# Optimization experiments

Measured on AMD Instinct MI355X. Metric: run time of the kernel, lower is better.

Reference implementation:

```python
import jax, jax.numpy as jnp
import numpy as np

HEAD_SIZE = 64
SCALE = HEAD_SIZE ** -0.5


def setup_inputs() -> dict:
    key = jax.random.key(0)
    ks = jax.random.split(key, 7)
    B, T, E, H = 32, 2048, 1024, HEAD_SIZE
    x = jax.random.normal(ks[0], (B, T, E), dtype=jnp.float32)
    Wq = jax.random.normal(ks[1], (E, H), dtype=jnp.float32) * (E ** -0.5)
    bq = jax.random.normal(ks[2], (H,), dtype=jnp.float32) * 0.02
    Wk = jax.random.normal(ks[3], (E, H), dtype=jnp.float32) * (E ** -0.5)
    bk = jax.random.normal(ks[4], (H,), dtype=jnp.float32) * 0.02
    Wv = jax.random.normal(ks[5], (E, H), dtype=jnp.float32) * (E ** -0.5)
    bv = jax.random.normal(ks[6], (H,), dtype=jnp.float32) * 0.02
    return {"x": x, "Wq": Wq, "bq": bq, "Wk": Wk, "bk": bk, "Wv": Wv, "bv": bv}


def reference(x, Wq, bq, Wk, bk, Wv, bv):
    # Faithful to the torch source: the tril buffer is all ones so the mask is a
    # no-op, and F.softmax's result is discarded. Output = (Q K^T * scale) @ V.
    Q = x @ Wq + bq          # [B, T, H]
    K = x @ Wk + bk          # [B, T, H]
    V = x @ Wv + bv          # [B, T, H]
    wei = jnp.einsum('bqh,bkh->bqk', Q, K) * SCALE  # [B, T, T]
    return jnp.einsum('bqk,bkh->bqh', wei, V)       # [B, T, H]
```

## Files before the change

kernel.cpp:

```cpp
#include <hip/hip_runtime.h>
#include <hip/hip_bf16.h>


using bf16x8 = __attribute__((ext_vector_type(8))) short;
using f32x4  = __attribute__((ext_vector_type(4))) float;
using u32x4  = __attribute__((ext_vector_type(4))) unsigned int;
using u32x2  = __attribute__((ext_vector_type(2))) unsigned int;
using u16    = unsigned short;

__device__ __forceinline__ u16 f2bf(float f) {
    unsigned u = __builtin_bit_cast(unsigned, f);
    u += 0x7fffu + ((u >> 16) & 1u);
    return (u16)(u >> 16);
}

#define G2L16(g, l) __builtin_amdgcn_global_load_lds(                         \
    (const __attribute__((address_space(1))) void*)(g),                       \
    (__attribute__((address_space(3))) void*)(l), 16, 0, 0)

__global__ __launch_bounds__(256) void k_wt(const float* __restrict__ Wq,
                                            const float* __restrict__ Wk,
                                            const float* __restrict__ Wv,
                                            u16* __restrict__ WT) {
    __shared__ float Wl[64][68];
    const int seg = blockIdx.x >> 4, chunk = blockIdx.x & 15;
    const float* W = (seg == 0) ? Wq : (seg == 1) ? Wk : Wv;
    const int e0 = chunk * 64;
    const int tid = threadIdx.x;
    const int lr = tid >> 4, lc = (tid & 15) * 4;
#pragma unroll
    for (int p = 0; p < 4; ++p)
        *(f32x4*)&Wl[lr + p * 16][lc] = *(const f32x4*)(W + (size_t)(e0 + lr + p * 16) * 64 + lc);
    __syncthreads();
    const int c = tid >> 2, eb = (tid & 3) * 16;
    u32x4 o0, o1;
#pragma unroll
    for (int q = 0; q < 4; ++q)
        o0[q] = (unsigned)f2bf(Wl[eb + 2 * q][c]) | ((unsigned)f2bf(Wl[eb + 2 * q + 1][c]) << 16);
#pragma unroll
    for (int q = 0; q < 4; ++q)
        o1[q] = (unsigned)f2bf(Wl[eb + 8 + 2 * q][c]) | ((unsigned)f2bf(Wl[eb + 9 + 2 * q][c]) << 16);
    u16* dst = WT + (size_t)(seg * 64 + c) * 1024 + e0 + eb;
    *(u32x4*)dst = o0;
    *(u32x4*)(dst + 8) = o1;
}

__global__ __launch_bounds__(512, 4) void k_qkv(const float* __restrict__ x,
                                                const u16* __restrict__ WT,
                                                const float* __restrict__ bq,
                                                const float* __restrict__ bk,
                                                const float* __restrict__ bv,
                                                u16* __restrict__ Qb,
                                                float* __restrict__ part) {
    __shared__ __align__(16) char lds[81920];
    const int tid  = threadIdx.x;
    const int wave = tid >> 6, lane = tid & 63;
    const int wr = wave >> 2, wc = wave & 3;
    const size_t row0 = (size_t)blockIdx.x * 64;

    size_t xsrc[2]; int xdst[2];
#pragma unroll
    for (int i = 0; i < 2; ++i) {
        const int r  = (tid >> 4) + i * 32;
        const int cb = ((tid & 15) * 16) ^ ((r & 7) << 5);
        xsrc[i] = (row0 + r) * 1024 + (cb >> 2);
        xdst[i] = i * 8192 + wave * 1024;
    }
    size_t wsrc[3]; int wdst[3];
#pragma unroll
    for (int j = 0; j < 3; ++j) {
        const int n  = (tid >> 3) + j * 64;
        const int cb = ((tid & 7) * 16) ^ ((n & 7) << 4);
        wsrc[j] = (size_t)n * 1024 + (cb >> 1);
        wdst[j] = 16384 + j * 8192 + wave * 1024;
    }

    f32x4 acc[2][3];
#pragma unroll
    for (int m = 0; m < 2; ++m)
#pragma unroll
        for (int n = 0; n < 3; ++n)
#pragma unroll
            for (int r = 0; r < 4; ++r) acc[m][n][r] = 0.0f;

#pragma unroll
    for (int i = 0; i < 2; ++i) G2L16(x + xsrc[i], lds + xdst[i]);
#pragma unroll
    for (int j = 0; j < 3; ++j) G2L16(WT + wsrc[j], lds + wdst[j]);

    for (int kc = 0; kc < 16; ++kc) {
        const int cur = kc & 1;
        if (kc < 15) {
            const int k0 = (kc + 1) * 64;
            char* base = lds + (cur ^ 1) * 40960;
#pragma unroll
            for (int i = 0; i < 2; ++i) G2L16(x + xsrc[i] + k0, base + xdst[i]);
#pragma unroll
            for (int j = 0; j < 3; ++j) G2L16(WT + wsrc[j] + k0, base + wdst[j]);
            asm volatile("s_waitcnt vmcnt(5)" ::: "memory");
        } else {
            asm volatile("s_waitcnt vmcnt(0)" ::: "memory");
        }
        __builtin_amdgcn_s_barrier();
        __builtin_amdgcn_sched_barrier(0);

        const char* xb = lds + cur * 40960;
        const char* wb = xb + 16384;
#pragma unroll
        for (int ks = 0; ks < 2; ++ks) {
            bf16x8 af[2];
#pragma unroll
            for (int m = 0; m < 2; ++m) {
                const int r = wr * 32 + m * 16 + (lane & 15);
                const int P = (r * 256 + ks * 128 + (lane >> 4) * 32) ^ ((r & 7) << 5);
                const f32x4 lo = *(const f32x4*)(xb + P);
                const f32x4 hi = *(const f32x4*)(xb + P + 16);
                u32x4 pk;
                pk[0] = (unsigned)f2bf(lo[0]) | ((unsigned)f2bf(lo[1]) << 16);
                pk[1] = (unsigned)f2bf(lo[2]) | ((unsigned)f2bf(lo[3]) << 16);
                pk[2] = (unsigned)f2bf(hi[0]) | ((unsigned)f2bf(hi[1]) << 16);
                pk[3] = (unsigned)f2bf(hi[2]) | ((unsigned)f2bf(hi[3]) << 16);
                af[m] = __builtin_bit_cast(bf16x8, pk);
            }
#pragma unroll
            for (int n = 0; n < 3; ++n) {
                const int nn = wc * 48 + n * 16 + (lane & 15);
                const int P  = (nn * 128 + ks * 64 + (lane >> 4) * 16) ^ ((nn & 7) << 4);
                const bf16x8 bfr = *(const bf16x8*)(wb + P);
                acc[0][n] = __builtin_amdgcn_mfma_f32_16x16x32_bf16(af[0], bfr, acc[0][n], 0, 0, 0);
                acc[1][n] = __builtin_amdgcn_mfma_f32_16x16x32_bf16(af[1], bfr, acc[1][n], 0, 0, 0);
            }
        }
        __builtin_amdgcn_sched_barrier(0);
        __builtin_amdgcn_s_barrier();
    }

    u16* const Kt = (u16*)lds;
    u16* const Vt = (u16*)(lds + 16384);
#pragma unroll
    for (int n = 0; n < 3; ++n) {
        const int ncol = wc * 48 + n * 16;
        const int seg = ncol >> 6;
        const int col = (ncol & 63) + (lane & 15);
        const float bias = ((seg == 0) ? bq : (seg == 1) ? bk : bv)[col];
#pragma unroll
        for (int m = 0; m < 2; ++m) {
            const int rloc = wr * 32 + m * 16 + ((lane >> 4) << 2);
            if (seg == 0) {
#pragma unroll
                for (int rr = 0; rr < 4; ++rr)
                    Qb[(row0 + rloc + rr) * 64 + col] = f2bf(acc[m][n][rr] + bias);
            } else {
                u16* const T = (seg == 1) ? Kt : Vt;
#pragma unroll
                for (int rr = 0; rr < 4; ++rr)
                    T[col * 72 + rloc + rr] = f2bf(acc[m][n][rr] + bias);
            }
        }
    }
    __syncthreads();

    float* const P = part + (size_t)blockIdx.x * 4096;
#pragma unroll
    for (int i = 0; i < 2; ++i) {
        const int f = wave * 2 + i;
        const int m0 = (f & 3) * 16;
        const int n0 = (f >> 2) * 16;
        f32x4 d;
        d[0] = d[1] = d[2] = d[3] = 0.0f;
#pragma unroll
        for (int ks = 0; ks < 2; ++ks) {
            const bf16x8 a = *(const bf16x8*)(Vt + (m0 + (lane & 15)) * 72 + ks * 32 + (lane >> 4) * 8);
            const bf16x8 b = *(const bf16x8*)(Kt + (n0 + (lane & 15)) * 72 + ks * 32 + (lane >> 4) * 8);
            d = __builtin_amdgcn_mfma_f32_16x16x32_bf16(a, b, d, 0, 0, 0);
        }
#pragma unroll
        for (int rr = 0; rr < 4; ++rr)
            P[(m0 + (lane >> 4) * 4 + rr) * 64 + n0 + (lane & 15)] = d[rr];
    }
}

__global__ __launch_bounds__(256) void k_red(const float* __restrict__ part,
                                             u16* __restrict__ KtVT) {
    const int b = blockIdx.x >> 2;
    const int o0 = (blockIdx.x & 3) * 1024 + threadIdx.x * 4;
    const float* const Pb = part + (size_t)b * 32 * 4096;
    f32x4 s;
    s[0] = s[1] = s[2] = s[3] = 0.0f;
#pragma unroll 8
    for (int c = 0; c < 32; ++c) s += *(const f32x4*)(Pb + c * 4096 + o0);
    s *= 0.125f;
    u32x2 pk;
    pk[0] = (unsigned)f2bf(s[0]) | ((unsigned)f2bf(s[1]) << 16);
    pk[1] = (unsigned)f2bf(s[2]) | ((unsigned)f2bf(s[3]) << 16);
    *(u32x2*)(KtVT + (size_t)b * 4096 + o0) = pk;
}

__global__ __launch_bounds__(256) void k_out(const u16* __restrict__ Qb,
                                             const u16* __restrict__ KtVT,
                                             float* __restrict__ out) {
    const int tid = threadIdx.x;
    const int wave = tid >> 6, lane = tid & 63;
    const size_t m0 = (size_t)blockIdx.x * 64 + wave * 16;
    const int b = blockIdx.x >> 5;
    const u16* const Bp = KtVT + (size_t)b * 4096;

    bf16x8 bfrag[2][4];
#pragma unroll
    for (int ks = 0; ks < 2; ++ks)
#pragma unroll
        for (int nt = 0; nt < 4; ++nt)
            bfrag[ks][nt] = *(const bf16x8*)(Bp + (nt * 16 + (lane & 15)) * 64 + ks * 32 + (lane >> 4) * 8);

    f32x4 acc[4];
#pragma unroll
    for (int nt = 0; nt < 4; ++nt)
#pragma unroll
        for (int r = 0; r < 4; ++r) acc[nt][r] = 0.0f;

#pragma unroll
    for (int ks = 0; ks < 2; ++ks) {
        const bf16x8 a = *(const bf16x8*)(Qb + (m0 + (lane & 15)) * 64 + ks * 32 + (lane >> 4) * 8);
#pragma unroll
        for (int nt = 0; nt < 4; ++nt)
            acc[nt] = __builtin_amdgcn_mfma_f32_16x16x32_bf16(a, bfrag[ks][nt], acc[nt], 0, 0, 0);
    }
#pragma unroll
    for (int nt = 0; nt < 4; ++nt)
#pragma unroll
        for (int rr = 0; rr < 4; ++rr)
            out[(m0 + (lane >> 4) * 4 + rr) * 64 + nt * 16 + (lane & 15)] = acc[nt][rr];
}

extern "C" void kernel_launch(void* const* d_in, const int* in_sizes, int n_in,
                              void* d_out, int out_size, void* d_ws, size_t ws_size,
                              hipStream_t stream) {
    (void)in_sizes; (void)n_in; (void)out_size; (void)ws_size;
    const float* x  = (const float*)d_in[0];
    const float* Wq = (const float*)d_in[1];
    const float* bq = (const float*)d_in[2];
    const float* Wk = (const float*)d_in[3];
    const float* bk = (const float*)d_in[4];
    const float* Wv = (const float*)d_in[5];
    const float* bv = (const float*)d_in[6];
    float* out = (float*)d_out;

    char* ws = (char*)d_ws;
    u16*  WT   = (u16*)(ws);
    u16*  Qb   = (u16*)(ws + 0x60000);
    float* part= (float*)(ws + 0x860000);
    u16*  KtVT = (u16*)(ws + 0x1860000);

    k_wt <<<48,   256, 0, stream>>>(Wq, Wk, Wv, WT);
    k_qkv<<<1024, 512, 0, stream>>>(x, WT, bq, bk, bv, Qb, part);
    k_red<<<128,  256, 0, stream>>>(part, KtVT);
    k_out<<<1024, 256, 0, stream>>>(Qb, KtVT, out);
}
```

Before: 92.33 us.

## Convert x to bf16 once in registers before staging in LDS for QKV GEMM

Rewrites the QKV projection mainloop so x is loaded into registers as fp32, converted to bf16 once, and stored into a larger bf16 LDS tile covering 256 K elements. This replaces fp32 staging via global_load_lds that re-converted each A fragment on every use. Weight tiles keep their own double-buffered async loads with adjusted waitcnts. LDS grows to 112 KB and occupancy drops to 2 blocks per CU, and the x loads are now synchronous register loads that need careful wait scheduling.

```diff
diff --git a/kernel.cpp b/kernel.cpp
--- a/kernel.cpp
+++ b/kernel.cpp
@@ -45,34 +45,30 @@
     *(u32x4*)(dst + 8) = o1;
 }
 
-__global__ __launch_bounds__(512, 4) void k_qkv(const float* __restrict__ x,
+__global__ __launch_bounds__(512, 2) void k_qkv(const float* __restrict__ x,
                                                 const u16* __restrict__ WT,
                                                 const float* __restrict__ bq,
                                                 const float* __restrict__ bk,
                                                 const float* __restrict__ bv,
                                                 u16* __restrict__ Qb,
                                                 float* __restrict__ part) {
-    __shared__ __align__(16) char lds[81920];
+    __shared__ __align__(16) char lds[114688];
     const int tid  = threadIdx.x;
     const int wave = tid >> 6, lane = tid & 63;
     const int wr = wave >> 2, wc = wave & 3;
     const size_t row0 = (size_t)blockIdx.x * 64;
 
-    size_t xsrc[2]; int xdst[2];
-#pragma unroll
-    for (int i = 0; i < 2; ++i) {
-        const int r  = (tid >> 4) + i * 32;
-        const int cb = ((tid & 15) * 16) ^ ((r & 7) << 5);
-        xsrc[i] = (row0 + r) * 1024 + (cb >> 2);
-        xdst[i] = i * 8192 + wave * 1024;
-    }
-    size_t wsrc[3]; int wdst[3];
+    const int xrow = tid >> 3;
+    const int xcs  = tid & 7;
+    const float* const xrowp = x + (row0 + xrow) * 1024 + xcs * 4;
+
+    size_t wsrc[3]; int wdstl[3];
 #pragma unroll
     for (int j = 0; j < 3; ++j) {
         const int n  = (tid >> 3) + j * 64;
         const int cb = ((tid & 7) * 16) ^ ((n & 7) << 4);
         wsrc[j] = (size_t)n * 1024 + (cb >> 1);
-        wdst[j] = 16384 + j * 8192 + wave * 1024;
+        wdstl[j] = j * 8192 + wave * 1024;
     }
 
     f32x4 acc[2][3];
@@ -83,56 +79,87 @@
 #pragma unroll
             for (int r = 0; r < 4; ++r) acc[m][n][r] = 0.0f;
 
-#pragma unroll
-    for (int i = 0; i < 2; ++i) G2L16(x + xsrc[i], lds + xdst[i]);
-#pragma unroll
-    for (int j = 0; j < 3; ++j) G2L16(WT + wsrc[j], lds + wdst[j]);
-
-    for (int kc = 0; kc < 16; ++kc) {
-        const int cur = kc & 1;
-        if (kc < 15) {
-            const int k0 = (kc + 1) * 64;
-            char* base = lds + (cur ^ 1) * 40960;
-#pragma unroll
-            for (int i = 0; i < 2; ++i) G2L16(x + xsrc[i] + k0, base + xdst[i]);
-#pragma unroll
-            for (int j = 0; j < 3; ++j) G2L16(WT + wsrc[j] + k0, base + wdst[j]);
-            asm volatile("s_waitcnt vmcnt(5)" ::: "memory");
-        } else {
-            asm volatile("s_waitcnt vmcnt(0)" ::: "memory");
-        }
-        __builtin_amdgcn_s_barrier();
-        __builtin_amdgcn_sched_barrier(0);
-
-        const char* xb = lds + cur * 40960;
-        const char* wb = xb + 16384;
-#pragma unroll
-        for (int ks = 0; ks < 2; ++ks) {
-            bf16x8 af[2];
-#pragma unroll
-            for (int m = 0; m < 2; ++m) {
-                const int r = wr * 32 + m * 16 + (lane & 15);
-                const int P = (r * 256 + ks * 128 + (lane >> 4) * 32) ^ ((r & 7) << 5);
-                const f32x4 lo = *(const f32x4*)(xb + P);
-                const f32x4 hi = *(const f32x4*)(xb + P + 16);
-                u32x4 pk;
-                pk[0] = (unsigned)f2bf(lo[0]) | ((unsigned)f2bf(lo[1]) << 16);
-                pk[1] = (unsigned)f2bf(lo[2]) | ((unsigned)f2bf(lo[3]) << 16);
-                pk[2] = (unsigned)f2bf(hi[0]) | ((unsigned)f2bf(hi[1]) << 16);
-                pk[3] = (unsigned)f2bf(hi[2]) | ((unsigned)f2bf(hi[3]) << 16);
-                af[m] = __builtin_bit_cast(bf16x8, pk);
-            }
-#pragma unroll
-            for (int n = 0; n < 3; ++n) {
-                const int nn = wc * 48 + n * 16 + (lane & 15);
-                const int P  = (nn * 128 + ks * 64 + (lane >> 4) * 16) ^ ((nn & 7) << 4);
-                const bf16x8 bfr = *(const bf16x8*)(wb + P);
-                acc[0][n] = __builtin_amdgcn_mfma_f32_16x16x32_bf16(af[0], bfr, acc[0][n], 0, 0, 0);
-                acc[1][n] = __builtin_amdgcn_mfma_f32_16x16x32_bf16(af[1], bfr, acc[1][n], 0, 0, 0);
-            }
-        }
-        __builtin_amdgcn_sched_barrier(0);
-        __builtin_amdgcn_s_barrier();
+    f32x4 xreg[8];
+
+#pragma unroll
+    for (int q = 0; q < 8; ++q) xreg[q] = *(const f32x4*)(xrowp + q * 32);
+    asm volatile("" ::: "memory");
+    __builtin_amdgcn_sched_barrier(0);
+#pragma unroll
+    for (int j = 0; j < 3; ++j) G2L16(WT + wsrc[j], lds + 65536 + wdstl[j]);
+    {
+        char* const xb = lds;
+#pragma unroll
+        for (int q = 0; q < 8; ++q) {
+            u32x2 pk;
+            pk[0] = (unsigned)f2bf(xreg[q][0]) | ((unsigned)f2bf(xreg[q][1]) << 16);
+            pk[1] = (unsigned)f2bf(xreg[q][2]) | ((unsigned)f2bf(xreg[q][3]) << 16);
+            *(u32x2*)(xb + ((xrow * 512 + q * 64 + xcs * 8) ^ ((xrow & 7) << 4))) = pk;
+        }
+    }
+    asm volatile("s_waitcnt lgkmcnt(0)" ::: "memory");
+    __builtin_amdgcn_s_barrier();
+
+#pragma unroll
+    for (int mk = 0; mk < 4; ++mk) {
+#pragma unroll
+        for (int c = 0; c < 4; ++c) {
+            const int ch = mk * 4 + c;
+            if (ch < 15) {
+                char* const wbase = lds + 65536 + ((ch + 1) & 1) * 24576;
+                const int k0 = (ch + 1) * 64;
+#pragma unroll
+                for (int j = 0; j < 3; ++j) G2L16(WT + wsrc[j] + k0, wbase + wdstl[j]);
+            }
+            if (c == 0 && mk < 3) {
+#pragma unroll
+                for (int q = 0; q < 8; ++q)
+                    xreg[q] = *(const f32x4*)(xrowp + (mk + 1) * 256 + q * 32);
+                asm volatile("" ::: "memory");
+                __builtin_amdgcn_sched_barrier(0);
+            }
+            if (c <= 1 && mk < 3)  asm volatile("s_waitcnt vmcnt(11)" ::: "memory");
+            else if (ch < 15)      asm volatile("s_waitcnt vmcnt(3)" ::: "memory");
+            else                   asm volatile("s_waitcnt vmcnt(0)" ::: "memory");
+            __builtin_amdgcn_s_barrier();
+            __builtin_amdgcn_sched_barrier(0);
+
+            {
+                const char* const xb = lds + (mk & 1) * 32768;
+                const char* const wb = lds + 65536 + (ch & 1) * 24576;
+#pragma unroll
+                for (int ks = 0; ks < 2; ++ks) {
+                    bf16x8 af[2];
+#pragma unroll
+                    for (int m = 0; m < 2; ++m) {
+                        const int r = wr * 32 + m * 16 + (lane & 15);
+                        const int P = (r * 512 + c * 128 + ks * 64 + (lane >> 4) * 16) ^ ((r & 7) << 4);
+                        af[m] = *(const bf16x8*)(xb + P);
+                    }
+#pragma unroll
+                    for (int n = 0; n < 3; ++n) {
+                        const int nn = wc * 48 + n * 16 + (lane & 15);
+                        const int P  = (nn * 128 + ks * 64 + (lane >> 4) * 16) ^ ((nn & 7) << 4);
+                        const bf16x8 bfr = *(const bf16x8*)(wb + P);
+                        acc[0][n] = __builtin_amdgcn_mfma_f32_16x16x32_bf16(af[0], bfr, acc[0][n], 0, 0, 0);
+                        acc[1][n] = __builtin_amdgcn_mfma_f32_16x16x32_bf16(af[1], bfr, acc[1][n], 0, 0, 0);
+                    }
+                }
+            }
+            if (c == 3 && mk < 3) {
+                char* const xb = lds + ((mk + 1) & 1) * 32768;
+#pragma unroll
+                for (int q = 0; q < 8; ++q) {
+                    u32x2 pk;
+                    pk[0] = (unsigned)f2bf(xreg[q][0]) | ((unsigned)f2bf(xreg[q][1]) << 16);
+                    pk[1] = (unsigned)f2bf(xreg[q][2]) | ((unsigned)f2bf(xreg[q][3]) << 16);
+                    *(u32x2*)(xb + ((xrow * 512 + q * 64 + xcs * 8) ^ ((xrow & 7) << 4))) = pk;
+                }
+                asm volatile("s_waitcnt lgkmcnt(0)" ::: "memory");
+            }
+            __builtin_amdgcn_sched_barrier(0);
+            __builtin_amdgcn_s_barrier();
+        }
     }
 
     u16* const Kt = (u16*)lds;
```

Result: slower. 110.2 us (+19.4%).

## Double QKV row tile to 128 and convert x to bf16 once in registers

Applied to the files above, without the earlier changes.

The QKV projection kernel now processes 128 rows per block instead of 64, so each W tile loaded into LDS is reused across twice as many rows and only half as many partial K^T V blocks have to be reduced. x is loaded through registers two stages ahead, converted to bf16 once and written to LDS as bf16. Previously it was staged as fp32 and converted per fragment read. This cuts LDS footprint and conversion work but raises register pressure (12 accumulators plus prefetch registers) and halves the grid to 512 blocks, which may lower occupancy.

```diff
diff --git a/kernel.cpp b/kernel.cpp
--- a/kernel.cpp
+++ b/kernel.cpp
@@ -55,91 +55,119 @@
     __shared__ __align__(16) char lds[81920];
     const int tid  = threadIdx.x;
     const int wave = tid >> 6, lane = tid & 63;
-    const int wr = wave >> 2, wc = wave & 3;
-    const size_t row0 = (size_t)blockIdx.x * 64;
-
-    size_t xsrc[2]; int xdst[2];
-#pragma unroll
-    for (int i = 0; i < 2; ++i) {
-        const int r  = (tid >> 4) + i * 32;
-        const int cb = ((tid & 15) * 16) ^ ((r & 7) << 5);
-        xsrc[i] = (row0 + r) * 1024 + (cb >> 2);
-        xdst[i] = i * 8192 + wave * 1024;
-    }
-    size_t wsrc[3]; int wdst[3];
+    const int wr = wave >> 1, wc = wave & 1;
+    const size_t row0 = (size_t)blockIdx.x * 128;
+
+    const int xr = tid >> 2, xc4 = tid & 3;
+    const float* const xp = x + (row0 + xr) * 1024 + xc4 * 16;
+    const int xw_b0 = (xr * 128 + xc4 * 32) ^ ((xr & 7) << 4);
+    const int xw_b1 = (xr * 128 + xc4 * 32 + 16) ^ ((xr & 7) << 4);
+
+    size_t wsrc[3]; int wdstl[3];
 #pragma unroll
     for (int j = 0; j < 3; ++j) {
         const int n  = (tid >> 3) + j * 64;
         const int cb = ((tid & 7) * 16) ^ ((n & 7) << 4);
         wsrc[j] = (size_t)n * 1024 + (cb >> 1);
-        wdst[j] = 16384 + j * 8192 + wave * 1024;
-    }
-
-    f32x4 acc[2][3];
+        wdstl[j] = j * 8192 + wave * 1024;
+    }
+
+    f32x4 acc[2][6];
 #pragma unroll
     for (int m = 0; m < 2; ++m)
 #pragma unroll
-        for (int n = 0; n < 3; ++n)
+        for (int n = 0; n < 6; ++n)
 #pragma unroll
             for (int r = 0; r < 4; ++r) acc[m][n][r] = 0.0f;
 
-#pragma unroll
-    for (int i = 0; i < 2; ++i) G2L16(x + xsrc[i], lds + xdst[i]);
-#pragma unroll
-    for (int j = 0; j < 3; ++j) G2L16(WT + wsrc[j], lds + wdst[j]);
-
-    for (int kc = 0; kc < 16; ++kc) {
-        const int cur = kc & 1;
-        if (kc < 15) {
-            const int k0 = (kc + 1) * 64;
-            char* base = lds + (cur ^ 1) * 40960;
-#pragma unroll
-            for (int i = 0; i < 2; ++i) G2L16(x + xsrc[i] + k0, base + xdst[i]);
-#pragma unroll
-            for (int j = 0; j < 3; ++j) G2L16(WT + wsrc[j] + k0, base + wdst[j]);
-            asm volatile("s_waitcnt vmcnt(5)" ::: "memory");
-        } else {
-            asm volatile("s_waitcnt vmcnt(0)" ::: "memory");
-        }
-        __builtin_amdgcn_s_barrier();
-        __builtin_amdgcn_sched_barrier(0);
-
-        const char* xb = lds + cur * 40960;
-        const char* wb = xb + 16384;
-#pragma unroll
-        for (int ks = 0; ks < 2; ++ks) {
-            bf16x8 af[2];
-#pragma unroll
-            for (int m = 0; m < 2; ++m) {
-                const int r = wr * 32 + m * 16 + (lane & 15);
-                const int P = (r * 256 + ks * 128 + (lane >> 4) * 32) ^ ((r & 7) << 5);
-                const f32x4 lo = *(const f32x4*)(xb + P);
-                const f32x4 hi = *(const f32x4*)(xb + P + 16);
-                u32x4 pk;
-                pk[0] = (unsigned)f2bf(lo[0]) | ((unsigned)f2bf(lo[1]) << 16);
-                pk[1] = (unsigned)f2bf(lo[2]) | ((unsigned)f2bf(lo[3]) << 16);
-                pk[2] = (unsigned)f2bf(hi[0]) | ((unsigned)f2bf(hi[1]) << 16);
-                pk[3] = (unsigned)f2bf(hi[2]) | ((unsigned)f2bf(hi[3]) << 16);
-                af[m] = __builtin_bit_cast(bf16x8, pk);
-            }
-#pragma unroll
-            for (int n = 0; n < 3; ++n) {
-                const int nn = wc * 48 + n * 16 + (lane & 15);
-                const int P  = (nn * 128 + ks * 64 + (lane >> 4) * 16) ^ ((nn & 7) << 4);
-                const bf16x8 bfr = *(const bf16x8*)(wb + P);
-                acc[0][n] = __builtin_amdgcn_mfma_f32_16x16x32_bf16(af[0], bfr, acc[0][n], 0, 0, 0);
-                acc[1][n] = __builtin_amdgcn_mfma_f32_16x16x32_bf16(af[1], bfr, acc[1][n], 0, 0, 0);
-            }
-        }
-        __builtin_amdgcn_sched_barrier(0);
-        __builtin_amdgcn_s_barrier();
+    f32x4 rA[4], rB[4];
+
+#define WRITE_X(BUF, R)                                                       \
+    {                                                                         \
+        char* const xbw_ = lds + (BUF) * 16384;                               \
+        u32x4 p0_, p1_;                                                       \
+        p0_[0] = (unsigned)f2bf(R[0][0]) | ((unsigned)f2bf(R[0][1]) << 16);   \
+        p0_[1] = (unsigned)f2bf(R[0][2]) | ((unsigned)f2bf(R[0][3]) << 16);   \
+        p0_[2] = (unsigned)f2bf(R[1][0]) | ((unsigned)f2bf(R[1][1]) << 16);   \
+        p0_[3] = (unsigned)f2bf(R[1][2]) | ((unsigned)f2bf(R[1][3]) << 16);   \
+        p1_[0] = (unsigned)f2bf(R[2][0]) | ((unsigned)f2bf(R[2][1]) << 16);   \
+        p1_[1] = (unsigned)f2bf(R[2][2]) | ((unsigned)f2bf(R[2][3]) << 16);   \
+        p1_[2] = (unsigned)f2bf(R[3][0]) | ((unsigned)f2bf(R[3][1]) << 16);   \
+        p1_[3] = (unsigned)f2bf(R[3][2]) | ((unsigned)f2bf(R[3][3]) << 16);   \
+        *(u32x4*)(xbw_ + xw_b0) = p0_;                                        \
+        *(u32x4*)(xbw_ + xw_b1) = p1_;                                        \
+    }
+
+#define COMPUTE(BUF)                                                          \
+    {                                                                         \
+        const char* const xb_ = lds + (BUF) * 16384;                          \
+        const char* const wb_ = lds + 32768 + (BUF) * 24576;                  \
+        _Pragma("unroll")                                                     \
+        for (int ks = 0; ks < 2; ++ks) {                                      \
+            bf16x8 af[2];                                                     \
+            _Pragma("unroll")                                                 \
+            for (int m = 0; m < 2; ++m) {                                     \
+                const int r_ = wr * 32 + m * 16 + (lane & 15);                \
+                af[m] = *(const bf16x8*)(xb_ +                                \
+                    ((r_ * 128 + ks * 64 + (lane >> 4) * 16) ^ ((r_ & 7) << 4))); \
+            }                                                                 \
+            _Pragma("unroll")                                                 \
+            for (int n = 0; n < 6; ++n) {                                     \
+                const int nn_ = wc * 96 + n * 16 + (lane & 15);               \
+                const bf16x8 bfr_ = *(const bf16x8*)(wb_ +                    \
+                    ((nn_ * 128 + ks * 64 + (lane >> 4) * 16) ^ ((nn_ & 7) << 4))); \
+                acc[0][n] = __builtin_amdgcn_mfma_f32_16x16x32_bf16(af[0], bfr_, acc[0][n], 0, 0, 0); \
+                acc[1][n] = __builtin_amdgcn_mfma_f32_16x16x32_bf16(af[1], bfr_, acc[1][n], 0, 0, 0); \
+            }                                                                 \
+        }                                                                     \
+    }
+
+#define PHASE(K, RN, RF)                                                      \
+    {                                                                         \
+        const int k_ = (K);                                                   \
+        if (k_ < 15) {                                                        \
+            char* const wbb_ = lds + 32768 + ((k_ + 1) & 1) * 24576;          \
+            const int k0_ = (k_ + 1) * 64;                                    \
+            _Pragma("unroll")                                                 \
+            for (int j = 0; j < 3; ++j) G2L16(WT + wsrc[j] + k0_, wbb_ + wdstl[j]); \
+        }                                                                     \
+        if (k_ < 14) {                                                        \
+            _Pragma("unroll")                                                 \
+            for (int q = 0; q < 4; ++q)                                       \
+                RF[q] = *(const f32x4*)(xp + (k_ + 2) * 64 + q * 4);          \
+        }                                                                     \
+        asm volatile("" ::: "memory");                                        \
+        if (k_ < 15) asm volatile("s_waitcnt vmcnt(7)" ::: "memory");         \
+        else         asm volatile("s_waitcnt vmcnt(0)" ::: "memory");         \
+        __builtin_amdgcn_s_barrier();                                         \
+        __builtin_amdgcn_sched_barrier(0);                                    \
+        if (k_ < 15) WRITE_X((k_ + 1) & 1, RN);                               \
+        COMPUTE(k_ & 1);                                                      \
+        asm volatile("s_waitcnt lgkmcnt(0)" ::: "memory");                    \
+        __builtin_amdgcn_sched_barrier(0);                                    \
+        __builtin_amdgcn_s_barrier();                                         \
+    }
+
+#pragma unroll
+    for (int q = 0; q < 4; ++q) rA[q] = *(const f32x4*)(xp + q * 4);
+#pragma unroll
+    for (int j = 0; j < 3; ++j) G2L16(WT + wsrc[j], lds + 32768 + wdstl[j]);
+#pragma unroll
+    for (int q = 0; q < 4; ++q) rB[q] = *(const f32x4*)(xp + 64 + q * 4);
+    asm volatile("s_waitcnt vmcnt(7)" ::: "memory");
+    WRITE_X(0, rA);
+    asm volatile("s_waitcnt lgkmcnt(0)" ::: "memory");
+
+    for (int kk = 0; kk < 16; kk += 2) {
+        PHASE(kk,     rB, rA);
+        PHASE(kk + 1, rA, rB);
     }
 
     u16* const Kt = (u16*)lds;
-    u16* const Vt = (u16*)(lds + 16384);
-#pragma unroll
-    for (int n = 0; n < 3; ++n) {
-        const int ncol = wc * 48 + n * 16;
+    u16* const Vt = (u16*)(lds + 20480);
+#pragma unroll
+    for (int n = 0; n < 6; ++n) {
+        const int ncol = wc * 96 + n * 16;
         const int seg = ncol >> 6;
         const int col = (ncol & 63) + (lane & 15);
         const float bias = ((seg == 0) ? bq : (seg == 1) ? bk : bv)[col];
@@ -154,7 +182,7 @@
                 u16* const T = (seg == 1) ? Kt : Vt;
 #pragma unroll
                 for (int rr = 0; rr < 4; ++rr)
-                    T[col * 72 + rloc + rr] = f2bf(acc[m][n][rr] + bias);
+                    T[col * 136 + rloc + rr] = f2bf(acc[m][n][rr] + bias);
             }
         }
     }
@@ -169,26 +197,29 @@
         f32x4 d;
         d[0] = d[1] = d[2] = d[3] = 0.0f;
 #pragma unroll
-        for (int ks = 0; ks < 2; ++ks) {
-            const bf16x8 a = *(const bf16x8*)(Vt + (m0 + (lane & 15)) * 72 + ks * 32 + (lane >> 4) * 8);
-            const bf16x8 b = *(const bf16x8*)(Kt + (n0 + (lane & 15)) * 72 + ks * 32 + (lane >> 4) * 8);
+        for (int ks = 0; ks < 4; ++ks) {
+            const bf16x8 a = *(const bf16x8*)(Vt + (m0 + (lane & 15)) * 136 + ks * 32 + (lane >> 4) * 8);
+            const bf16x8 b = *(const bf16x8*)(Kt + (n0 + (lane & 15)) * 136 + ks * 32 + (lane >> 4) * 8);
             d = __builtin_amdgcn_mfma_f32_16x16x32_bf16(a, b, d, 0, 0, 0);
         }
 #pragma unroll
         for (int rr = 0; rr < 4; ++rr)
             P[(m0 + (lane >> 4) * 4 + rr) * 64 + n0 + (lane & 15)] = d[rr];
     }
+#undef PHASE
+#undef COMPUTE
+#undef WRITE_X
 }
 
 __global__ __launch_bounds__(256) void k_red(const float* __restrict__ part,
                                              u16* __restrict__ KtVT) {
     const int b = blockIdx.x >> 2;
     const int o0 = (blockIdx.x & 3) * 1024 + threadIdx.x * 4;
-    const float* const Pb = part + (size_t)b * 32 * 4096;
+    const float* const Pb = part + (size_t)b * 16 * 4096;
     f32x4 s;
     s[0] = s[1] = s[2] = s[3] = 0.0f;
 #pragma unroll 8
-    for (int c = 0; c < 32; ++c) s += *(const f32x4*)(Pb + c * 4096 + o0);
+    for (int c = 0; c < 16; ++c) s += *(const f32x4*)(Pb + c * 4096 + o0);
     s *= 0.125f;
     u32x2 pk;
     pk[0] = (unsigned)f2bf(s[0]) | ((unsigned)f2bf(s[1]) << 16);
@@ -249,10 +280,10 @@
     u16*  WT   = (u16*)(ws);
     u16*  Qb   = (u16*)(ws + 0x60000);
     float* part= (float*)(ws + 0x860000);
-    u16*  KtVT = (u16*)(ws + 0x1860000);
+    u16*  KtVT = (u16*)(ws + 0x1060000);
 
     k_wt <<<48,   256, 0, stream>>>(Wq, Wk, Wv, WT);
-    k_qkv<<<1024, 512, 0, stream>>>(x, WT, bq, bk, bv, Qb, part);
+    k_qkv<<<512,  512, 0, stream>>>(x, WT, bq, bk, bv, Qb, part);
     k_red<<<128,  256, 0, stream>>>(part, KtVT);
     k_out<<<1024, 256, 0, stream>>>(Qb, KtVT, out);
 }
```

Result: slower. 143.7 us (+55.7%).

## Restructure QKV projection: 4 waves, triple-buffered x tiles, weights read directly from global

Applied to the files above, without the earlier changes.

The QKV projection kernel moves from 8 waves to 4 waves per block, and each wave now computes 6 output column tiles instead of 3. Only x tiles are staged through LDS, using a three-deep ring with prefetch distance two and a single barrier per k-step. Weight fragments are loaded straight from global memory (expected to hit L2) instead of LDS. This cuts LDS footprint and barrier count and deepens prefetch, but adds register pressure and uncoalesced direct global loads for the weights in the inner loop.

```diff
diff --git a/kernel.cpp b/kernel.cpp
--- a/kernel.cpp
+++ b/kernel.cpp
@@ -45,74 +45,61 @@
     *(u32x4*)(dst + 8) = o1;
 }
 
-__global__ __launch_bounds__(512, 4) void k_qkv(const float* __restrict__ x,
+__global__ __launch_bounds__(256, 3) void k_qkv(const float* __restrict__ x,
                                                 const u16* __restrict__ WT,
                                                 const float* __restrict__ bq,
                                                 const float* __restrict__ bk,
                                                 const float* __restrict__ bv,
                                                 u16* __restrict__ Qb,
                                                 float* __restrict__ part) {
-    __shared__ __align__(16) char lds[81920];
+    __shared__ __align__(16) char lds[49152];
     const int tid  = threadIdx.x;
     const int wave = tid >> 6, lane = tid & 63;
-    const int wr = wave >> 2, wc = wave & 3;
+    const int wr = wave >> 1, wc = wave & 1;
     const size_t row0 = (size_t)blockIdx.x * 64;
 
-    size_t xsrc[2]; int xdst[2];
-#pragma unroll
-    for (int i = 0; i < 2; ++i) {
-        const int r  = (tid >> 4) + i * 32;
-        const int cb = ((tid & 15) * 16) ^ ((r & 7) << 5);
-        xsrc[i] = (row0 + r) * 1024 + (cb >> 2);
-        xdst[i] = i * 8192 + wave * 1024;
-    }
-    size_t wsrc[3]; int wdst[3];
-#pragma unroll
-    for (int j = 0; j < 3; ++j) {
-        const int n  = (tid >> 3) + j * 64;
-        const int cb = ((tid & 7) * 16) ^ ((n & 7) << 4);
-        wsrc[j] = (size_t)n * 1024 + (cb >> 1);
-        wdst[j] = 16384 + j * 8192 + wave * 1024;
-    }
-
-    f32x4 acc[2][3];
+    size_t xsrc[4]; int xdst[4];
+#pragma unroll
+    for (int i = 0; i < 4; ++i) {
+        const int r    = wave * 16 + i * 4 + (lane >> 4);
+        const int csrc = ((lane & 15) * 4) ^ ((r & 7) << 3);
+        xsrc[i] = (row0 + r) * 1024 + csrc;
+        xdst[i] = wave * 4096 + i * 1024;
+    }
+
+    f32x4 acc[2][6];
 #pragma unroll
     for (int m = 0; m < 2; ++m)
 #pragma unroll
-        for (int n = 0; n < 3; ++n)
+        for (int n = 0; n < 6; ++n)
 #pragma unroll
             for (int r = 0; r < 4; ++r) acc[m][n][r] = 0.0f;
 
 #pragma unroll
-    for (int i = 0; i < 2; ++i) G2L16(x + xsrc[i], lds + xdst[i]);
-#pragma unroll
-    for (int j = 0; j < 3; ++j) G2L16(WT + wsrc[j], lds + wdst[j]);
-
-    for (int kc = 0; kc < 16; ++kc) {
-        const int cur = kc & 1;
-        if (kc < 15) {
-            const int k0 = (kc + 1) * 64;
-            char* base = lds + (cur ^ 1) * 40960;
-#pragma unroll
-            for (int i = 0; i < 2; ++i) G2L16(x + xsrc[i] + k0, base + xdst[i]);
-#pragma unroll
-            for (int j = 0; j < 3; ++j) G2L16(WT + wsrc[j] + k0, base + wdst[j]);
-            asm volatile("s_waitcnt vmcnt(5)" ::: "memory");
-        } else {
-            asm volatile("s_waitcnt vmcnt(0)" ::: "memory");
-        }
+    for (int i = 0; i < 4; ++i) G2L16(x + xsrc[i], lds + xdst[i]);
+#pragma unroll
+    for (int i = 0; i < 4; ++i) G2L16(x + xsrc[i] + 64, lds + 16384 + xdst[i]);
+
+    for (int k = 0; k < 16; ++k) {
+        if (k < 15) asm volatile("s_waitcnt vmcnt(4)" ::: "memory");
+        else        asm volatile("s_waitcnt vmcnt(0)" ::: "memory");
         __builtin_amdgcn_s_barrier();
-        __builtin_amdgcn_sched_barrier(0);
-
-        const char* xb = lds + cur * 40960;
-        const char* wb = xb + 16384;
+        if (k + 2 < 16) {
+            char* const dbuf = lds + ((k + 2) % 3) * 16384;
+            const int k0 = (k + 2) * 64;
+#pragma unroll
+            for (int i = 0; i < 4; ++i) G2L16(x + xsrc[i] + k0, dbuf + xdst[i]);
+        }
+
+        const char* const xb = lds + (k % 3) * 16384;
+        const u16* const wk = WT + k * 64;
 #pragma unroll
         for (int ks = 0; ks < 2; ++ks) {
             bf16x8 af[2];
 #pragma unroll
             for (int m = 0; m < 2; ++m) {
-                const int r = wr * 32 + m * 16 + (lane & 15);
-                const int P = (r * 256 + ks * 128 + (lane >> 4) * 32) ^ ((r & 7) << 5);
+                const int r_ = wr * 32 + m * 16 + (lane & 15);
+                const int P  = (r_ * 256 + ks * 128 + (lane >> 4) * 32) ^ ((r_ & 7) << 5);
                 const f32x4 lo = *(const f32x4*)(xb + P);
                 const f32x4 hi = *(const f32x4*)(xb + P + 16);
                 u32x4 pk;
@@ -123,23 +110,21 @@
                 af[m] = __builtin_bit_cast(bf16x8, pk);
             }
 #pragma unroll
-            for (int n = 0; n < 3; ++n) {
-                const int nn = wc * 48 + n * 16 + (lane & 15);
-                const int P  = (nn * 128 + ks * 64 + (lane >> 4) * 16) ^ ((nn & 7) << 4);
-                const bf16x8 bfr = *(const bf16x8*)(wb + P);
+            for (int n = 0; n < 6; ++n) {
+                const int nn = wc * 96 + n * 16 + (lane & 15);
+                const bf16x8 bfr = *(const bf16x8*)(wk + (size_t)nn * 1024 + ks * 32 + (lane >> 4) * 8);
                 acc[0][n] = __builtin_amdgcn_mfma_f32_16x16x32_bf16(af[0], bfr, acc[0][n], 0, 0, 0);
                 acc[1][n] = __builtin_amdgcn_mfma_f32_16x16x32_bf16(af[1], bfr, acc[1][n], 0, 0, 0);
             }
         }
-        __builtin_amdgcn_sched_barrier(0);
-        __builtin_amdgcn_s_barrier();
-    }
+    }
+    __syncthreads();
 
     u16* const Kt = (u16*)lds;
-    u16* const Vt = (u16*)(lds + 16384);
-#pragma unroll
-    for (int n = 0; n < 3; ++n) {
-        const int ncol = wc * 48 + n * 16;
+    u16* const Vt = (u16*)(lds + 10240);
+#pragma unroll
+    for (int n = 0; n < 6; ++n) {
+        const int ncol = wc * 96 + n * 16;
         const int seg = ncol >> 6;
         const int col = (ncol & 63) + (lane & 15);
         const float bias = ((seg == 0) ? bq : (seg == 1) ? bk : bv)[col];
@@ -162,8 +147,8 @@
 
     float* const P = part + (size_t)blockIdx.x * 4096;
 #pragma unroll
-    for (int i = 0; i < 2; ++i) {
-        const int f = wave * 2 + i;
+    for (int i = 0; i < 4; ++i) {
+        const int f = wave * 4 + i;
         const int m0 = (f & 3) * 16;
         const int n0 = (f >> 2) * 16;
         f32x4 d;
@@ -252,7 +237,7 @@
     u16*  KtVT = (u16*)(ws + 0x1860000);
 
     k_wt <<<48,   256, 0, stream>>>(Wq, Wk, Wv, WT);
-    k_qkv<<<1024, 512, 0, stream>>>(x, WT, bq, bk, bv, Qb, part);
+    k_qkv<<<1024, 256, 0, stream>>>(x, WT, bq, bk, bv, Qb, part);
     k_red<<<128,  256, 0, stream>>>(part, KtVT);
     k_out<<<1024, 256, 0, stream>>>(Qb, KtVT, out);
 }
```

Measured after the change: 186.8 us. 2.02x slower.
